# Kernel tuning notes

Measured on AMD Instinct MI355X. Metric: run time of the kernel, lower is better.

Reference implementation:

```python
import jax, jax.numpy as jnp
import numpy as np

B, S, D = 128, 256, 768          # batch, seq (pre-sentinel), encoder dim
ARC, TAG = 500, 100              # arc / tag representation dims
LAYERS, TOPK = 2, 8              # config['gnn_layers'], config['top_k']
SP = S + 1                       # seq_len after head sentinel


def setup_inputs() -> dict:
    key = jax.random.key(0)
    ks = jax.random.split(key, 32)
    sc = 0.02
    inp = {
        'inputs': jax.random.normal(ks[0], (B, S, D), jnp.float32),
        'tag_embeddings': jax.random.randint(ks[1], (B, S), 0, 50),
        'mask': jnp.ones((B, S), jnp.int32),
        'head_indices': jax.random.randint(ks[2], (B, S), 0, S),
        'head_tags': jax.random.randint(ks[3], (B, S), 0, 50),
        # parameters
        'head_sentinel': jax.random.normal(ks[4], (D,), jnp.float32),
        'W_ha': jax.random.normal(ks[5], (D, ARC)) * sc, 'b_ha': jnp.zeros((ARC,)),
        'W_da': jax.random.normal(ks[6], (D, ARC)) * sc, 'b_da': jnp.zeros((ARC,)),
        'W_ht': jax.random.normal(ks[7], (D, TAG)) * sc, 'b_ht': jnp.zeros((TAG,)),
        'W_dt': jax.random.normal(ks[8], (D, TAG)) * sc, 'b_dt': jnp.zeros((TAG,)),
        # bilinear attention: use_input_biases=True -> (ARC+1, ARC+1), plus scalar bias
        'bil_W': jax.random.normal(ks[9], (LAYERS + 1, ARC + 1, ARC + 1)) * sc,
        'bil_b': jnp.zeros((LAYERS + 1,)),
        # GCNConv params (PyG: x @ W, symmetric-normalized aggregate, + bias)
        'c1a_W': jax.random.normal(ks[10], (ARC, ARC)) * sc, 'c1a_b': jnp.zeros((ARC,)),
        'c2a_W': jax.random.normal(ks[11], (ARC, ARC)) * sc, 'c2a_b': jnp.zeros((ARC,)),
        'c1r_W': jax.random.normal(ks[12], (TAG, TAG)) * sc, 'c1r_b': jnp.zeros((TAG,)),
        'c2r_W': jax.random.normal(ks[13], (TAG, TAG)) * sc, 'c2r_b': jnp.zeros((TAG,)),
    }
    return inp


def bilinear_attn(m1, m2, W, b):
    # AllenNLP BilinearMatrixAttention with use_input_biases=True
    ones1 = jnp.ones(m1.shape[:-1] + (1,), m1.dtype)
    m1b = jnp.concatenate([m1, ones1], -1)
    m2b = jnp.concatenate([m2, ones1], -1)
    return jnp.einsum('bie,ef,bjf->bij', m1b, W, m2b) + b


def batch_top_k(probs, k):
    # probs: [B, SP, SP] row-softmaxed; edge j(head)->i(dep) for each row's top-k cols,
    # with global (batched) node indexing.
    vals, idx = jax.lax.top_k(probs, k)                      # [B, SP, k]
    offs = (jnp.arange(B) * SP)[:, None, None]
    src = (idx + offs).reshape(-1)
    dst = (jnp.broadcast_to(jnp.arange(SP)[None, :, None], idx.shape) + offs).reshape(-1)
    return src, dst, vals.reshape(-1)


def gcn_conv(x, src, dst, ew, W, b):
    # PyG GCNConv: x@W, add self-loops (weight 1), sym norm, scatter-add at dst, + bias
    N = x.shape[0]
    x = x @ W
    loop = jnp.arange(N)
    row = jnp.concatenate([src, loop])
    col = jnp.concatenate([dst, loop])
    w = jnp.concatenate([ew, jnp.ones((N,), x.dtype)])
    deg = jax.ops.segment_sum(w, col, num_segments=N)
    dinv = jnp.where(deg > 0, jax.lax.rsqrt(deg), 0.0)
    norm = dinv[row] * w * dinv[col]
    out = jax.ops.segment_sum(x[row] * norm[:, None], col, num_segments=N)
    return out + b


def reference(inputs, tag_embeddings, mask, head_indices, head_tags,
              head_sentinel, W_ha, b_ha, W_da, b_da, W_ht, b_ht, W_dt, b_dt,
              bil_W, bil_b, c1a_W, c1a_b, c2a_W, c2a_b, c1r_W, c1r_b, c2r_W, c2r_b):
    elu = jax.nn.elu
    x = jnp.concatenate([jnp.broadcast_to(head_sentinel, (B, 1, D)), inputs], axis=1)  # [B,SP,D]
    head_arc = elu(x @ W_ha + b_ha)
    dept_arc = elu(x @ W_da + b_da)
    head_tag = elu(x @ W_ht + b_ht)
    dep_tag = elu(x @ W_dt + b_dt)

    def two_conv(feat, W1, b1, W2, b2, src, dst, ew):
        h = gcn_conv(feat.reshape(B * SP, -1), src, dst, ew, W1, b1)
        h = gcn_conv(elu(h), src, dst, ew, W2, b2)
        return h.reshape(B, SP, -1)

    for k in range(LAYERS):
        arc_logits = bilinear_attn(head_arc, dept_arc, bil_W[k], bil_b[k])
        arc_probs = jax.nn.softmax(arc_logits, axis=-1)
        src, dst, ew = batch_top_k(arc_probs, TOPK)
        head_arc = two_conv(head_arc, c1a_W, c1a_b, c2a_W, c2a_b, src, dst, ew)
        dept_arc = two_conv(dept_arc, c1a_W, c1a_b, c2a_W, c2a_b, src, dst, ew)
        head_tag = two_conv(head_tag, c1r_W, c1r_b, c2r_W, c2r_b, src, dst, ew)
        dep_tag = two_conv(dep_tag, c1r_W, c1r_b, c2r_W, c2r_b, src, dst, ew)

    arc_logits = bilinear_attn(head_arc, dept_arc, bil_W[-1], bil_b[-1])
    return arc_logits, head_tag, dep_tag
```

## Files before the change

kernel.cpp:

```cpp
#include <hip/hip_runtime.h>
#include <hip/hip_bf16.h>
#include <math.h>
#include <cstddef>

namespace {

constexpr int kB   = 128;
constexpr int kS   = 256;
constexpr int kD   = 768;
constexpr int kSP  = 257;
constexpr int kN   = kB * kSP;
constexpr int kARC = 500;
constexpr int kTAG = 100;
constexpr int KA   = 512;
constexpr int KT   = 128;

typedef __attribute__((ext_vector_type(8))) short short8;
typedef __attribute__((ext_vector_type(4))) float floatx4;

__device__ __forceinline__ float bfval(__hip_bfloat16 h) { return __bfloat162float(h); }
__device__ __forceinline__ float s2f(short s) {
  unsigned short us = (unsigned short)s;
  __hip_bfloat16 h;
  __builtin_memcpy(&h, &us, 2);
  return __bfloat162float(h);
}
__device__ __forceinline__ void splitf(float x, __hip_bfloat16* h, __hip_bfloat16* l) {
  __hip_bfloat16 hh = __float2bfloat16(x);
  *h = hh;
  *l = __float2bfloat16(x - __bfloat162float(hh));
}

__global__ void detect_dtype_n(const unsigned* __restrict__ raw, int* __restrict__ flag,
                               int nwords) {
  int lane = threadIdx.x;
  int ok = 0, nz = 0;
  if (lane < nwords) {
    unsigned w = raw[lane];
    if (w != 0u) {
      nz = 1;
      int e = (w >> 7) & 0xFF;
      ok = (e >= 90 && e <= 140);
    }
  }
  unsigned long long ball_ok = __ballot(ok);
  unsigned long long ball_nz = __ballot(nz);
  if (lane == 0) {
    int cok = __popcll(ball_ok), cnz = __popcll(ball_nz);
    flag[0] = (cok * 4 >= cnz * 3) ? 1 : 0;
  }
}

__device__ __forceinline__ float rawload(const void* p, size_t i, int bf) {
  return bf ? __bfloat162float(((const __hip_bfloat16*)p)[i]) : ((const float*)p)[i];
}

__global__ void conv_off(const void* __restrict__ src, float* __restrict__ dst,
                         int n, long off, const int* __restrict__ flag) {
  int i = blockIdx.x * 256 + threadIdx.x;
  if (i >= n) return;
  dst[i] = rawload(src, (size_t)off + i, *flag);
}

__global__ void wsplit_t(const void* __restrict__ src, const int* __restrict__ flag,
                         long srcOff, int ldsrc, int K, int N, int Kpad,
                         __hip_bfloat16* __restrict__ Wh, __hip_bfloat16* __restrict__ Wl) {
  long idx = (long)blockIdx.x * 256 + threadIdx.x;
  if (idx >= (long)N * Kpad) return;
  int n = (int)(idx / Kpad), k = (int)(idx % Kpad);
  float v = (k < K) ? rawload(src, (size_t)srcOff + (size_t)k * ldsrc + n, *flag) : 0.f;
  __hip_bfloat16 h, l;
  splitf(v, &h, &l);
  Wh[idx] = h; Wl[idx] = l;
}

constexpr int BM = 128, BN = 128, BK = 32, LDT = 40;

template <int EPI>
__global__ __launch_bounds__(256) void gemm_sp(
    const __hip_bfloat16* __restrict__ Ah, const __hip_bfloat16* __restrict__ Al, int lda,
    const __hip_bfloat16* __restrict__ Bh, const __hip_bfloat16* __restrict__ Bl, int ldb,
    __hip_bfloat16* __restrict__ Ch, __hip_bfloat16* __restrict__ Cl, int ldc,
    int M, int N, int K, const float* __restrict__ bias) {
  __shared__ __hip_bfloat16 sA[2][BM][LDT];
  __shared__ __hip_bfloat16 sB[2][BN][LDT];
  const int tid = threadIdx.x;
  const int lane = tid & 63, wave = tid >> 6;
  const int quad = lane >> 4, l15 = lane & 15;
  const int wm = (wave >> 1) * 64, wn = (wave & 1) * 64;
  const int m0 = blockIdx.x * BM, n0 = blockIdx.y * BN;
  const int srow = tid >> 2, sck = tid & 3;

  floatx4 acc[4][4] = {};
  for (int k0 = 0; k0 < K; k0 += BK) {
#pragma unroll
    for (int half = 0; half < 2; ++half) {
      int r = srow + half * 64;
      {
        int gm = m0 + r;
        short8 vh = {}, vl = {};
        if (gm < M) {
          vh = *(const short8*)(Ah + (size_t)gm * lda + k0 + sck * 8);
          vl = *(const short8*)(Al + (size_t)gm * lda + k0 + sck * 8);
        }
        *(short8*)&sA[0][r][sck * 8] = vh;
        *(short8*)&sA[1][r][sck * 8] = vl;
      }
      {
        int gn = n0 + r;
        short8 vh = {}, vl = {};
        if (gn < N) {
          vh = *(const short8*)(Bh + (size_t)gn * ldb + k0 + sck * 8);
          vl = *(const short8*)(Bl + (size_t)gn * ldb + k0 + sck * 8);
        }
        *(short8*)&sB[0][r][sck * 8] = vh;
        *(short8*)&sB[1][r][sck * 8] = vl;
      }
    }
    __syncthreads();
    short8 a_h[4], a_l[4], b_h[4], b_l[4];
#pragma unroll
    for (int t = 0; t < 4; ++t) {
      a_h[t] = *(const short8*)&sA[0][wm + t * 16 + l15][quad * 8];
      a_l[t] = *(const short8*)&sA[1][wm + t * 16 + l15][quad * 8];
      b_h[t] = *(const short8*)&sB[0][wn + t * 16 + l15][quad * 8];
      b_l[t] = *(const short8*)&sB[1][wn + t * 16 + l15][quad * 8];
    }
#pragma unroll
    for (int mt = 0; mt < 4; ++mt)
#pragma unroll
      for (int nt = 0; nt < 4; ++nt) {
        acc[mt][nt] = __builtin_amdgcn_mfma_f32_16x16x32_bf16(a_h[mt], b_h[nt], acc[mt][nt], 0, 0, 0);
        acc[mt][nt] = __builtin_amdgcn_mfma_f32_16x16x32_bf16(a_h[mt], b_l[nt], acc[mt][nt], 0, 0, 0);
        acc[mt][nt] = __builtin_amdgcn_mfma_f32_16x16x32_bf16(a_l[mt], b_h[nt], acc[mt][nt], 0, 0, 0);
      }
    __syncthreads();
  }
#pragma unroll
  for (int mt = 0; mt < 4; ++mt)
#pragma unroll
    for (int reg = 0; reg < 4; ++reg) {
      int m = m0 + wm + mt * 16 + quad * 4 + reg;
      if (m >= M) continue;
#pragma unroll
      for (int nt = 0; nt < 4; ++nt) {
        int n = n0 + wn + nt * 16 + l15;
        size_t o = (size_t)m * ldc + n;
        if (n < N) {
          float v = acc[mt][nt][reg];
          if (EPI >= 1) v += bias[n];
          if (EPI == 1) v = v > 0.f ? v : expm1f(v);
          __hip_bfloat16 h, l;
          splitf(v, &h, &l);
          Ch[o] = h; Cl[o] = l;
        } else if (n < ldc) {
          Ch[o] = __float2bfloat16(0.f);
          Cl[o] = __float2bfloat16(0.f);
        }
      }
    }
}

__global__ __launch_bounds__(256) void proj_sp(
    const void* __restrict__ inp, const void* __restrict__ sent,
    const int* __restrict__ flag_inp, const int* __restrict__ flag_sent,
    const __hip_bfloat16* __restrict__ Bh, const __hip_bfloat16* __restrict__ Bl,
    __hip_bfloat16* __restrict__ Ch, __hip_bfloat16* __restrict__ Cl, int ldc,
    int M, int N, const float* __restrict__ bias, int g0) {
  __shared__ __hip_bfloat16 sA[2][BM][LDT];
  __shared__ __hip_bfloat16 sB[2][BN][LDT];
  const int bf_i = *flag_inp, bf_s = *flag_sent;
  const int tid = threadIdx.x;
  const int lane = tid & 63, wave = tid >> 6;
  const int quad = lane >> 4, l15 = lane & 15;
  const int wm = (wave >> 1) * 64, wn = (wave & 1) * 64;
  const int m0 = blockIdx.x * BM, n0 = blockIdx.y * BN;
  const int srow = tid >> 2, sck = tid & 3;

  floatx4 acc[4][4] = {};
  for (int k0 = 0; k0 < kD; k0 += BK) {
#pragma unroll
    for (int half = 0; half < 2; ++half) {
      int r = srow + half * 64;
      int gm = m0 + r;
      float v[8] = {0, 0, 0, 0, 0, 0, 0, 0};
      if (gm < M) {
        int b_loc = gm / kSP;
        int rr = gm - b_loc * kSP;
        int kk = k0 + sck * 8;
        if (rr == 0) {
          if (bf_s) {
            short8 s = *(const short8*)((const __hip_bfloat16*)sent + kk);
#pragma unroll
            for (int j = 0; j < 8; ++j) v[j] = s2f(s[j]);
          } else {
            floatx4 a = *(const floatx4*)((const float*)sent + kk);
            floatx4 b = *(const floatx4*)((const float*)sent + kk + 4);
#pragma unroll
            for (int j = 0; j < 4; ++j) { v[j] = a[j]; v[4 + j] = b[j]; }
          }
        } else {
          size_t base = ((size_t)((g0 + b_loc) * kS + (rr - 1))) * kD + kk;
          if (bf_i) {
            short8 s = *(const short8*)((const __hip_bfloat16*)inp + base);
#pragma unroll
            for (int j = 0; j < 8; ++j) v[j] = s2f(s[j]);
          } else {
            floatx4 a = *(const floatx4*)((const float*)inp + base);
            floatx4 b = *(const floatx4*)((const float*)inp + base + 4);
#pragma unroll
            for (int j = 0; j < 4; ++j) { v[j] = a[j]; v[4 + j] = b[j]; }
          }
        }
      }
#pragma unroll
      for (int j = 0; j < 8; ++j) {
        __hip_bfloat16 h, l;
        splitf(v[j], &h, &l);
        sA[0][r][sck * 8 + j] = h;
        sA[1][r][sck * 8 + j] = l;
      }
      {
        int gn = n0 + r;
        short8 vh = {}, vl = {};
        if (gn < N) {
          vh = *(const short8*)(Bh + (size_t)gn * kD + k0 + sck * 8);
          vl = *(const short8*)(Bl + (size_t)gn * kD + k0 + sck * 8);
        }
        *(short8*)&sB[0][r][sck * 8] = vh;
        *(short8*)&sB[1][r][sck * 8] = vl;
      }
    }
    __syncthreads();
    short8 a_h[4], a_l[4], b_h[4], b_l[4];
#pragma unroll
    for (int t = 0; t < 4; ++t) {
      a_h[t] = *(const short8*)&sA[0][wm + t * 16 + l15][quad * 8];
      a_l[t] = *(const short8*)&sA[1][wm + t * 16 + l15][quad * 8];
      b_h[t] = *(const short8*)&sB[0][wn + t * 16 + l15][quad * 8];
      b_l[t] = *(const short8*)&sB[1][wn + t * 16 + l15][quad * 8];
    }
#pragma unroll
    for (int mt = 0; mt < 4; ++mt)
#pragma unroll
      for (int nt = 0; nt < 4; ++nt) {
        acc[mt][nt] = __builtin_amdgcn_mfma_f32_16x16x32_bf16(a_h[mt], b_h[nt], acc[mt][nt], 0, 0, 0);
        acc[mt][nt] = __builtin_amdgcn_mfma_f32_16x16x32_bf16(a_h[mt], b_l[nt], acc[mt][nt], 0, 0, 0);
        acc[mt][nt] = __builtin_amdgcn_mfma_f32_16x16x32_bf16(a_l[mt], b_h[nt], acc[mt][nt], 0, 0, 0);
      }
    __syncthreads();
  }
#pragma unroll
  for (int mt = 0; mt < 4; ++mt)
#pragma unroll
    for (int reg = 0; reg < 4; ++reg) {
      int m = m0 + wm + mt * 16 + quad * 4 + reg;
      if (m >= M) continue;
#pragma unroll
      for (int nt = 0; nt < 4; ++nt) {
        int n = n0 + wn + nt * 16 + l15;
        size_t o = (size_t)m * ldc + n;
        if (n < N) {
          float v = acc[mt][nt][reg] + bias[n];
          v = v > 0.f ? v : expm1f(v);
          __hip_bfloat16 h, l;
          splitf(v, &h, &l);
          Ch[o] = h; Cl[o] = l;
        } else if (n < ldc) {
          Ch[o] = __float2bfloat16(0.f);
          Cl[o] = __float2bfloat16(0.f);
        }
      }
    }
}

__global__ __launch_bounds__(256) void bilnt_sp(
    const __hip_bfloat16* __restrict__ Th, const __hip_bfloat16* __restrict__ Tl,
    const __hip_bfloat16* __restrict__ Fh, const __hip_bfloat16* __restrict__ Fl,
    float* __restrict__ out, const float* __restrict__ bilb, int bidx,
    int g0, int globOut) {
  __shared__ __hip_bfloat16 sA[2][BM][LDT];
  __shared__ __hip_bfloat16 sB[2][BN][LDT];
  const int z = blockIdx.z;
  const int tid = threadIdx.x;
  const int lane = tid & 63, wave = tid >> 6;
  const int quad = lane >> 4, l15 = lane & 15;
  const int wm = (wave >> 1) * 64, wn = (wave & 1) * 64;
  const int m0 = blockIdx.x * BM, n0 = blockIdx.y * BN;
  const int srow = tid >> 2, sck = tid & 3;
  const __hip_bfloat16* Ah = Th + (size_t)z * kSP * KA;
  const __hip_bfloat16* Al = Tl + (size_t)z * kSP * KA;
  const __hip_bfloat16* Bh = Fh + (size_t)z * kSP * KA;
  const __hip_bfloat16* Bl = Fl + (size_t)z * kSP * KA;

  floatx4 acc[4][4] = {};
  for (int k0 = 0; k0 < KA; k0 += BK) {
#pragma unroll
    for (int half = 0; half < 2; ++half) {
      int r = srow + half * 64;
      {
        int gm = m0 + r;
        short8 vh = {}, vl = {};
        if (gm < kSP) {
          vh = *(const short8*)(Ah + (size_t)gm * KA + k0 + sck * 8);
          vl = *(const short8*)(Al + (size_t)gm * KA + k0 + sck * 8);
        }
        *(short8*)&sA[0][r][sck * 8] = vh;
        *(short8*)&sA[1][r][sck * 8] = vl;
      }
      {
        int gn = n0 + r;
        short8 vh = {}, vl = {};
        if (gn < kSP) {
          vh = *(const short8*)(Bh + (size_t)gn * KA + k0 + sck * 8);
          vl = *(const short8*)(Bl + (size_t)gn * KA + k0 + sck * 8);
        }
        *(short8*)&sB[0][r][sck * 8] = vh;
        *(short8*)&sB[1][r][sck * 8] = vl;
      }
    }
    __syncthreads();
    short8 a_h[4], a_l[4], b_h[4], b_l[4];
#pragma unroll
    for (int t = 0; t < 4; ++t) {
      a_h[t] = *(const short8*)&sA[0][wm + t * 16 + l15][quad * 8];
      a_l[t] = *(const short8*)&sA[1][wm + t * 16 + l15][quad * 8];
      b_h[t] = *(const short8*)&sB[0][wn + t * 16 + l15][quad * 8];
      b_l[t] = *(const short8*)&sB[1][wn + t * 16 + l15][quad * 8];
    }
#pragma unroll
    for (int mt = 0; mt < 4; ++mt)
#pragma unroll
      for (int nt = 0; nt < 4; ++nt) {
        acc[mt][nt] = __builtin_amdgcn_mfma_f32_16x16x32_bf16(a_h[mt], b_h[nt], acc[mt][nt], 0, 0, 0);
        acc[mt][nt] = __builtin_amdgcn_mfma_f32_16x16x32_bf16(a_h[mt], b_l[nt], acc[mt][nt], 0, 0, 0);
        acc[mt][nt] = __builtin_amdgcn_mfma_f32_16x16x32_bf16(a_l[mt], b_h[nt], acc[mt][nt], 0, 0, 0);
      }
    __syncthreads();
  }
  const float sb = bilb[bidx];
  const int bb = globOut ? (g0 + z) : z;
#pragma unroll
  for (int mt = 0; mt < 4; ++mt)
// ... 47 lines not shown
      float ov = __shfl_xor(bvv, off);
      int oi = __shfl_xor(bii, off);
      if (ov > bvv || (ov == bvv && oi < bii)) { bvv = ov; bii = oi; }
    }
    float p = expf(bvv - m) * invs;
    degsum += p;
    if (lane == 0) { idx8[row * 8 + t] = rowbase + bii; val8[row * 8 + t] = p; }
#pragma unroll
    for (int q = 0; q < 5; ++q)
      if (c[q] == bii) v[q] = -INFINITY;
  }
  if (lane == 0) dinv[row] = 1.f / sqrtf(1.f + degsum);
}

template <int ELU, int OUTF32>
__global__ __launch_bounds__(256) void gcn_agg_sp(
    const __hip_bfloat16* __restrict__ Yh, const __hip_bfloat16* __restrict__ Yl, int ldy,
    int F,
    const int* __restrict__ idx8, const float* __restrict__ val8,
    const float* __restrict__ dinv,
    const float* __restrict__ bias,
    __hip_bfloat16* __restrict__ Zh, __hip_bfloat16* __restrict__ Zl,
    float* __restrict__ Zf, int ldzf) {
  const int n = blockIdx.x;
  __shared__ float w[9];
  __shared__ int srcs[8];
  const int t = threadIdx.x;
  if (t < 8) {
    int s = idx8[n * 8 + t];
    srcs[t] = s;
    w[t] = dinv[n] * val8[n * 8 + t] * dinv[s];
  } else if (t == 8) {
    float di = dinv[n];
    w[8] = di * di;
  }
  __syncthreads();
  const int lim = OUTF32 ? F : ldy;
  for (int f = t; f < lim; f += blockDim.x) {
    if (!OUTF32 && f >= F) {
      size_t o = (size_t)n * ldy + f;
      Zh[o] = __float2bfloat16(0.f);
      Zl[o] = __float2bfloat16(0.f);
      continue;
    }
    size_t off0 = (size_t)n * ldy + f;
    float acc = w[8] * (bfval(Yh[off0]) + bfval(Yl[off0]));
#pragma unroll
    for (int k = 0; k < 8; ++k) {
      size_t o = (size_t)srcs[k] * ldy + f;
      acc += w[k] * (bfval(Yh[o]) + bfval(Yl[o]));
    }
    acc += bias[f];
    if (ELU) acc = acc > 0.f ? acc : expm1f(acc);
    if (OUTF32) {
      Zf[(size_t)n * ldzf + f] = acc;
    } else {
      __hip_bfloat16 h, l;
      splitf(acc, &h, &l);
      size_t o = (size_t)n * ldy + f;
      Zh[o] = h; Zl[o] = l;
    }
  }
}

}

extern "C" void kernel_launch(void* const* d_in, const int* in_sizes, int n_in,
                              void* d_out, int out_size, void* d_ws, size_t ws_size,
                              hipStream_t stream) {
  (void)out_size;

  const int roleSize[20] = {kB * kS * kD, kD,
                            kD * kARC, kARC, kD * kARC, kARC,
                            kD * kTAG, kTAG, kD * kTAG, kTAG,
                            3 * 501 * 501, 3,
// ... 17 lines not shown
  const void* src_of[20];
  for (int r = 0; r < 20; ++r) src_of[r] = d_in[roleIdx[r]];

  auto need_bytes = [](int GB) -> size_t {
    size_t NG = (size_t)GB * kSP, s = 0;
    auto al = [&](size_t b) { s += (b + 255) & ~(size_t)255; };
    al(256);
    for (int i = 0; i < 4; ++i) al((size_t)kARC * kD * 2);
    for (int i = 0; i < 4; ++i) al((size_t)kTAG * kD * 2);
    al(kARC * 4); al(kARC * 4); al(kTAG * 4); al(kTAG * 4);
    for (int i = 0; i < 6; ++i) al((size_t)501 * KA * 2);
    al(3 * 501 * 4); al(256);
    for (int i = 0; i < 4; ++i) al((size_t)kARC * KA * 2);
    for (int i = 0; i < 4; ++i) al((size_t)kTAG * KT * 2);
    al(kARC * 4); al(kARC * 4); al(kTAG * 4); al(kTAG * 4);
    for (int i = 0; i < 4; ++i) al(NG * KA * 2);
    for (int i = 0; i < 4; ++i) al(NG * KT * 2);
    for (int i = 0; i < 4; ++i) al(NG * KA * 2);
    al(NG * kSP * 4);
    al(NG * 8 * 4); al(NG * 8 * 4); al(NG * 4);
    return s;
  };
  int GB = 1;
  for (int cand : {128, 64, 32, 16, 8, 4, 2, 1})
    if (need_bytes(cand) <= ws_size) { GB = cand; break; }
  const int G = kB / GB;
  const int NG = GB * kSP;
  const int mb = (NG + BM - 1) / BM;

  char* ws = (char*)d_ws;
  size_t off = 0;
  auto alloc = [&](size_t bytes) -> void* {
    void* p = ws + off;
    off += (bytes + 255) & ~(size_t)255;
    return p;
  };
  typedef __hip_bfloat16 bf;
  int* flags = (int*)alloc(256);
  bf *WtHAh = (bf*)alloc((size_t)kARC * kD * 2), *WtHAl = (bf*)alloc((size_t)kARC * kD * 2);
  bf *WtDAh = (bf*)alloc((size_t)kARC * kD * 2), *WtDAl = (bf*)alloc((size_t)kARC * kD * 2);
  bf *WtHTh = (bf*)alloc((size_t)kTAG * kD * 2), *WtHTl = (bf*)alloc((size_t)kTAG * kD * 2);
  bf *WtDTh = (bf*)alloc((size_t)kTAG * kD * 2), *WtDTl = (bf*)alloc((size_t)kTAG * kD * 2);
  float* bha = (float*)alloc(kARC * 4);
  float* bda = (float*)alloc(kARC * 4);
  float* bht = (float*)alloc(kTAG * 4);
  float* bdt = (float*)alloc(kTAG * 4);
  bf* bilWh[3]; bf* bilWl[3];
  for (int k = 0; k < 3; ++k) {
    bilWh[k] = (bf*)alloc((size_t)501 * KA * 2);
    bilWl[k] = (bf*)alloc((size_t)501 * KA * 2);
  }
  float* brow = (float*)alloc(3 * 501 * 4);
  float* bilbf = (float*)alloc(256);
  bf *c1ah = (bf*)alloc((size_t)kARC * KA * 2), *c1al = (bf*)alloc((size_t)kARC * KA * 2);
  bf *c2ah = (bf*)alloc((size_t)kARC * KA * 2), *c2al = (bf*)alloc((size_t)kARC * KA * 2);
  bf *c1rh = (bf*)alloc((size_t)kTAG * KT * 2), *c1rl = (bf*)alloc((size_t)kTAG * KT * 2);
  bf *c2rh = (bf*)alloc((size_t)kTAG * KT * 2), *c2rl = (bf*)alloc((size_t)kTAG * KT * 2);
  float* c1ab = (float*)alloc(kARC * 4);
  float* c2ab = (float*)alloc(kARC * 4);
  float* c1rb = (float*)alloc(kTAG * 4);
  float* c2rb = (float*)alloc(kTAG * 4);
  bf *fHAh = (bf*)alloc((size_t)NG * KA * 2), *fHAl = (bf*)alloc((size_t)NG * KA * 2);
  bf *fDAh = (bf*)alloc((size_t)NG * KA * 2), *fDAl = (bf*)alloc((size_t)NG * KA * 2);
  bf *fHTh = (bf*)alloc((size_t)NG * KT * 2), *fHTl = (bf*)alloc((size_t)NG * KT * 2);
  bf *fDTh = (bf*)alloc((size_t)NG * KT * 2), *fDTl = (bf*)alloc((size_t)NG * KT * 2);
  bf *Yh = (bf*)alloc((size_t)NG * KA * 2), *Yl = (bf*)alloc((size_t)NG * KA * 2);
  bf *Zh = (bf*)alloc((size_t)NG * KA * 2), *Zl = (bf*)alloc((size_t)NG * KA * 2);
  float* logits = (float*)alloc((size_t)NG * kSP * 4);
  int*   idx8 = (int*)alloc((size_t)NG * 8 * 4);
  float* val8 = (float*)alloc((size_t)NG * 8 * 4);
  float* dinv = (float*)alloc((size_t)NG * 4);

  for (int r = 0; r < 20; ++r) {
    int n = roleSize[r];
    int nwords = n / 4; if (nwords < 1) nwords = 1; if (nwords > 64) nwords = 64;
    detect_dtype_n<<<1, 64, 0, stream>>>((const unsigned*)src_of[r], flags + r, nwords);
  }
  auto cvt = [&](int role, float* dst, int n, long o) {
    conv_off<<<(n + 255) / 256, 256, 0, stream>>>(src_of[role], dst, n, o, flags + role);
  };
  cvt(3, bha, kARC, 0); cvt(5, bda, kARC, 0); cvt(7, bht, kTAG, 0); cvt(9, bdt, kTAG, 0);
  cvt(11, bilbf, 3, 0);
// ... 10 lines not shown
  for (int k = 0; k < 3; ++k) {
    wsp(10, (long)k * 501 * 501, 501, 500, 501, KA, bilWh[k], bilWl[k]);
    cvt(10, brow + k * 501, 501, (long)k * 501 * 501 + 500 * 501);
  }
  wsp(12, 0, kARC, kARC, kARC, KA, c1ah, c1al);
  wsp(14, 0, kARC, kARC, kARC, KA, c2ah, c2al);
  wsp(16, 0, kTAG, kTAG, kTAG, KT, c1rh, c1rl);
  wsp(18, 0, kTAG, kTAG, kTAG, KT, c2rh, c2rl);

  float* outp = (float*)d_out;
  const size_t arc_elems = (size_t)kB * kSP * kSP;

  for (int g = 0; g < G; ++g) {
    const int g0 = g * GB;

    proj_sp<<<dim3(mb, 4), 256, 0, stream>>>(src_of[0], src_of[1], flags + 0, flags + 1,
                                             WtHAh, WtHAl, fHAh, fHAl, KA, NG, kARC, bha, g0);
    proj_sp<<<dim3(mb, 4), 256, 0, stream>>>(src_of[0], src_of[1], flags + 0, flags + 1,
                                             WtDAh, WtDAl, fDAh, fDAl, KA, NG, kARC, bda, g0);
    proj_sp<<<dim3(mb, 1), 256, 0, stream>>>(src_of[0], src_of[1], flags + 0, flags + 1,
                                             WtHTh, WtHTl, fHTh, fHTl, KT, NG, kTAG, bht, g0);
    proj_sp<<<dim3(mb, 1), 256, 0, stream>>>(src_of[0], src_of[1], flags + 0, flags + 1,
                                             WtDTh, WtDTl, fDTh, fDTl, KT, NG, kTAG, bdt, g0);

    for (int k = 0; k < 2; ++k) {
      gemm_sp<2><<<dim3(mb, 4), 256, 0, stream>>>(fHAh, fHAl, KA, bilWh[k], bilWl[k], KA,
                                                  Yh, Yl, KA, NG, 501, KA, brow + k * 501);
      bilnt_sp<<<dim3(3, 3, GB), 256, 0, stream>>>(Yh, Yl, fDAh, fDAl, logits, bilbf, k, g0, 0);
      softmax_topk<<<NG, 64, 0, stream>>>(logits, idx8, val8, dinv);

      bf* fh[2] = {fHAh, fDAh};
      bf* fl[2] = {fHAl, fDAl};
      for (int ff = 0; ff < 2; ++ff) {
        gemm_sp<0><<<dim3(mb, 4), 256, 0, stream>>>(fh[ff], fl[ff], KA, c1ah, c1al, KA,
                                                    Yh, Yl, KA, NG, kARC, KA, nullptr);
        gcn_agg_sp<1, 0><<<NG, 256, 0, stream>>>(Yh, Yl, KA, kARC, idx8, val8, dinv, c1ab,
                                                 Zh, Zl, nullptr, 0);
        gemm_sp<0><<<dim3(mb, 4), 256, 0, stream>>>(Zh, Zl, KA, c2ah, c2al, KA,
                                                    Yh, Yl, KA, NG, kARC, KA, nullptr);
        gcn_agg_sp<0, 0><<<NG, 256, 0, stream>>>(Yh, Yl, KA, kARC, idx8, val8, dinv, c2ab,
                                                 fh[ff], fl[ff], nullptr, 0);
      }
      bf* th[2] = {fHTh, fDTh};
      bf* tl[2] = {fHTl, fDTl};
      for (int ff = 0; ff < 2; ++ff) {
        gemm_sp<0><<<dim3(mb, 1), 256, 0, stream>>>(th[ff], tl[ff], KT, c1rh, c1rl, KT,
                                                    Zh, Zl, KT, NG, kTAG, KT, nullptr);
        gcn_agg_sp<1, 0><<<NG, 256, 0, stream>>>(Zh, Zl, KT, kTAG, idx8, val8, dinv, c1rb,
                                                 Yh, Yl, nullptr, 0);
        gemm_sp<0><<<dim3(mb, 1), 256, 0, stream>>>(Yh, Yl, KT, c2rh, c2rl, KT,
                                                    Zh, Zl, KT, NG, kTAG, KT, nullptr);
        if (k == 1) {
          float* dst = outp + arc_elems + (ff == 1 ? (size_t)kN * kTAG : 0)
                       + (size_t)g0 * kSP * kTAG;
          gcn_agg_sp<0, 1><<<NG, 256, 0, stream>>>(Zh, Zl, KT, kTAG, idx8, val8, dinv, c2rb,
                                                   nullptr, nullptr, dst, kTAG);
        } else {
          gcn_agg_sp<0, 0><<<NG, 256, 0, stream>>>(Zh, Zl, KT, kTAG, idx8, val8, dinv, c2rb,
                                                   th[ff], tl[ff], nullptr, 0);
        }
      }
    }

    gemm_sp<2><<<dim3(mb, 4), 256, 0, stream>>>(fHAh, fHAl, KA, bilWh[2], bilWl[2], KA,
                                                Yh, Yl, KA, NG, 501, KA, brow + 2 * 501);
    bilnt_sp<<<dim3(3, 3, GB), 256, 0, stream>>>(Yh, Yl, fDAh, fDAl, outp, bilbf, 2, g0, 1);
  }
}
```

Before: 3.163 ms.

## Use direct global-to-LDS loads, pre-split inputs, and fp32 intermediates for GCN

GEMM and bilinear kernels now stage tiles with global_load_lds (16-byte direct-to-LDS) into unpadded shared arrays, replacing register round-trips and bounds zeroing with clamped row pointers. The fused projection kernel is replaced by a one-time xsplit pass that converts the input to hi/lo bf16, followed by the generic GEMM. GCN transform GEMMs write fp32 outputs consumed by a rewritten aggregation kernel, and the tag-path aggregation uses 64-thread blocks. The unpadded LDS layout may cause bank conflicts on fragment reads, and the extra split buffer adds memory traffic.

```diff
diff --git a/kernel.cpp b/kernel.cpp
--- a/kernel.cpp
+++ b/kernel.cpp
@@ -17,18 +17,25 @@
 
 typedef __attribute__((ext_vector_type(8))) short short8;
 typedef __attribute__((ext_vector_type(4))) float floatx4;
-
-__device__ __forceinline__ float bfval(__hip_bfloat16 h) { return __bfloat162float(h); }
-__device__ __forceinline__ float s2f(short s) {
-  unsigned short us = (unsigned short)s;
-  __hip_bfloat16 h;
-  __builtin_memcpy(&h, &us, 2);
-  return __bfloat162float(h);
-}
-__device__ __forceinline__ void splitf(float x, __hip_bfloat16* h, __hip_bfloat16* l) {
-  __hip_bfloat16 hh = __float2bfloat16(x);
+typedef __attribute__((ext_vector_type(2))) float floatx2;
+typedef __attribute__((ext_vector_type(4))) unsigned short ushort4v;
+typedef __attribute__((ext_vector_type(2))) unsigned short ushort2v;
+typedef __hip_bfloat16 bf;
+
+__device__ __forceinline__ float bfval(bf h) { return __bfloat162float(h); }
+__device__ __forceinline__ unsigned short bfbits(bf h) {
+  unsigned short u; __builtin_memcpy(&u, &h, 2); return u;
+}
+__device__ __forceinline__ void splitf(float x, bf* h, bf* l) {
+  bf hh = __float2bfloat16(x);
   *h = hh;
   *l = __float2bfloat16(x - __bfloat162float(hh));
+}
+
+__device__ __forceinline__ void gload16(const bf* g, bf* l) {
+  __builtin_amdgcn_global_load_lds(
+      (const __attribute__((address_space(1))) void*)g,
+      (__attribute__((address_space(3))) void*)l, 16, 0, 0);
 }
 
 __global__ void detect_dtype_n(const unsigned* __restrict__ raw, int* __restrict__ flag,
@@ -51,8 +58,8 @@
   }
 }
 
-__device__ __forceinline__ float rawload(const void* p, size_t i, int bf) {
-  return bf ? __bfloat162float(((const __hip_bfloat16*)p)[i]) : ((const float*)p)[i];
+__device__ __forceinline__ float rawload(const void* p, size_t i, int bfm) {
+  return bfm ? __bfloat162float(((const bf*)p)[i]) : ((const float*)p)[i];
 }
 
 __global__ void conv_off(const void* __restrict__ src, float* __restrict__ dst,
@@ -64,67 +71,109 @@
 
 __global__ void wsplit_t(const void* __restrict__ src, const int* __restrict__ flag,
                          long srcOff, int ldsrc, int K, int N, int Kpad,
-                         __hip_bfloat16* __restrict__ Wh, __hip_bfloat16* __restrict__ Wl) {
+                         bf* __restrict__ Wh, bf* __restrict__ Wl) {
   long idx = (long)blockIdx.x * 256 + threadIdx.x;
   if (idx >= (long)N * Kpad) return;
   int n = (int)(idx / Kpad), k = (int)(idx % Kpad);
   float v = (k < K) ? rawload(src, (size_t)srcOff + (size_t)k * ldsrc + n, *flag) : 0.f;
-  __hip_bfloat16 h, l;
+  bf h, l;
   splitf(v, &h, &l);
   Wh[idx] = h; Wl[idx] = l;
 }
 
-constexpr int BM = 128, BN = 128, BK = 32, LDT = 40;
-
-template <int EPI>
+__global__ void xsplit(const void* __restrict__ inp, const void* __restrict__ sent,
+                       const int* __restrict__ fi, const int* __restrict__ fs,
+                       bf* __restrict__ xh, bf* __restrict__ xl, int g0, int NG) {
+  long idx = (long)blockIdx.x * 256 + threadIdx.x;
+  long tot = (long)NG * (kD / 4);
+  if (idx >= tot) return;
+  int n = (int)(idx / (kD / 4));
+  int k = (int)(idx % (kD / 4)) * 4;
+  int b = n / kSP, r = n - b * kSP;
+  const void* src;
+  size_t base;
+  int bfm;
+  if (r == 0) { src = sent; base = (size_t)k; bfm = *fs; }
+  else {
+    src = inp;
+    base = ((size_t)((g0 + b) * kS + (r - 1))) * kD + k;
+    bfm = *fi;
+  }
+  float v[4];
+  if (bfm) {
+    ushort4v s = *(const ushort4v*)((const unsigned short*)src + base);
+#pragma unroll
+    for (int j = 0; j < 4; ++j) {
+      bf h; unsigned short u = s[j];
+      __builtin_memcpy(&h, &u, 2);
+      v[j] = __bfloat162float(h);
+    }
+  } else {
+    floatx4 f4 = *(const floatx4*)((const float*)src + base);
+#pragma unroll
+    for (int j = 0; j < 4; ++j) v[j] = f4[j];
+  }
+  ushort4v h4, l4;
+#pragma unroll
+  for (int j = 0; j < 4; ++j) {
+    bf h, l;
+    splitf(v[j], &h, &l);
+    h4[j] = bfbits(h); l4[j] = bfbits(l);
+  }
+  size_t o = (size_t)n * kD + k;
+  *(ushort4v*)((unsigned short*)xh + o) = h4;
+  *(ushort4v*)((unsigned short*)xl + o) = l4;
+}
+
+constexpr int BM = 128, BN = 128, BK = 32;
+
+template <int EPI, int OUTF32>
 __global__ __launch_bounds__(256) void gemm_sp(
-    const __hip_bfloat16* __restrict__ Ah, const __hip_bfloat16* __restrict__ Al, int lda,
-    const __hip_bfloat16* __restrict__ Bh, const __hip_bfloat16* __restrict__ Bl, int ldb,
-    __hip_bfloat16* __restrict__ Ch, __hip_bfloat16* __restrict__ Cl, int ldc,
+    const bf* __restrict__ Ah, const bf* __restrict__ Al, int lda,
+    const bf* __restrict__ Bh, const bf* __restrict__ Bl, int ldb,
+    bf* __restrict__ Ch, bf* __restrict__ Cl, float* __restrict__ Cf, int ldc,
     int M, int N, int K, const float* __restrict__ bias) {
-  __shared__ __hip_bfloat16 sA[2][BM][LDT];
-  __shared__ __hip_bfloat16 sB[2][BN][LDT];
+  __shared__ bf sAh[BM][BK];
+  __shared__ bf sAl[BM][BK];
+  __shared__ bf sBh[BN][BK];
+  __shared__ bf sBl[BN][BK];
   const int tid = threadIdx.x;
   const int lane = tid & 63, wave = tid >> 6;
   const int quad = lane >> 4, l15 = lane & 15;
   const int wm = (wave >> 1) * 64, wn = (wave & 1) * 64;
   const int m0 = blockIdx.x * BM, n0 = blockIdx.y * BN;
-  const int srow = tid >> 2, sck = tid & 3;
+  const int lrow = lane >> 2, lkof = (lane & 3) * 8;
+
+  const bf *pAh[2], *pAl[2], *pBh[2], *pBl[2];
+#pragma unroll
+  for (int jj = 0; jj < 2; ++jj) {
+    int rb = wave * 32 + jj * 16;
+    int gm = m0 + rb + lrow; if (gm > M - 1) gm = M - 1;
+    int gn = n0 + rb + lrow; if (gn > N - 1) gn = N - 1;
+    pAh[jj] = Ah + (size_t)gm * lda + lkof;
+    pAl[jj] = Al + (size_t)gm * lda + lkof;
+    pBh[jj] = Bh + (size_t)gn * ldb + lkof;
+    pBl[jj] = Bl + (size_t)gn * ldb + lkof;
+  }
 
   floatx4 acc[4][4] = {};
   for (int k0 = 0; k0 < K; k0 += BK) {
 #pragma unroll
-    for (int half = 0; half < 2; ++half) {
-      int r = srow + half * 64;
-      {
-        int gm = m0 + r;
-        short8 vh = {}, vl = {};
-        if (gm < M) {
-          vh = *(const short8*)(Ah + (size_t)gm * lda + k0 + sck * 8);
-          vl = *(const short8*)(Al + (size_t)gm * lda + k0 + sck * 8);
-        }
-        *(short8*)&sA[0][r][sck * 8] = vh;
-        *(short8*)&sA[1][r][sck * 8] = vl;
-      }
-      {
-        int gn = n0 + r;
-        short8 vh = {}, vl = {};
-        if (gn < N) {
-          vh = *(const short8*)(Bh + (size_t)gn * ldb + k0 + sck * 8);
-          vl = *(const short8*)(Bl + (size_t)gn * ldb + k0 + sck * 8);
-        }
-        *(short8*)&sB[0][r][sck * 8] = vh;
-        *(short8*)&sB[1][r][sck * 8] = vl;
-      }
+    for (int jj = 0; jj < 2; ++jj) {
+      const int rb = wave * 32 + jj * 16;
+      gload16(pAh[jj] + k0, &sAh[rb][0]);
+      gload16(pAl[jj] + k0, &sAl[rb][0]);
+      gload16(pBh[jj] + k0, &sBh[rb][0]);
+      gload16(pBl[jj] + k0, &sBl[rb][0]);
     }
     __syncthreads();
     short8 a_h[4], a_l[4], b_h[4], b_l[4];
 #pragma unroll
     for (int t = 0; t < 4; ++t) {
-      a_h[t] = *(const short8*)&sA[0][wm + t * 16 + l15][quad * 8];
-      a_l[t] = *(const short8*)&sA[1][wm + t * 16 + l15][quad * 8];
-      b_h[t] = *(const short8*)&sB[0][wn + t * 16 + l15][quad * 8];
-      b_l[t] = *(const short8*)&sB[1][wn + t * 16 + l15][quad * 8];
+      a_h[t] = *(const short8*)&sAh[wm + t * 16 + l15][quad * 8];
+      a_l[t] = *(const short8*)&sAl[wm + t * 16 + l15][quad * 8];
+      b_h[t] = *(const short8*)&sBh[wn + t * 16 + l15][quad * 8];
+      b_l[t] = *(const short8*)&sBl[wn + t * 16 + l15][quad * 8];
     }
 #pragma unroll
     for (int mt = 0; mt < 4; ++mt)
@@ -145,188 +194,82 @@
 #pragma unroll
       for (int nt = 0; nt < 4; ++nt) {
         int n = n0 + wn + nt * 16 + l15;
-        size_t o = (size_t)m * ldc + n;
-        if (n < N) {
-          float v = acc[mt][nt][reg];
-          if (EPI >= 1) v += bias[n];
-          if (EPI == 1) v = v > 0.f ? v : expm1f(v);
-          __hip_bfloat16 h, l;
-          splitf(v, &h, &l);
-          Ch[o] = h; Cl[o] = l;
-        } else if (n < ldc) {
-          Ch[o] = __float2bfloat16(0.f);
-          Cl[o] = __float2bfloat16(0.f);
-        }
-      }
-    }
-}
-
-__global__ __launch_bounds__(256) void proj_sp(
-    const void* __restrict__ inp, const void* __restrict__ sent,
-    const int* __restrict__ flag_inp, const int* __restrict__ flag_sent,
-    const __hip_bfloat16* __restrict__ Bh, const __hip_bfloat16* __restrict__ Bl,
-    __hip_bfloat16* __restrict__ Ch, __hip_bfloat16* __restrict__ Cl, int ldc,
-    int M, int N, const float* __restrict__ bias, int g0) {
-  __shared__ __hip_bfloat16 sA[2][BM][LDT];
-  __shared__ __hip_bfloat16 sB[2][BN][LDT];
-  const int bf_i = *flag_inp, bf_s = *flag_sent;
-  const int tid = threadIdx.x;
-  const int lane = tid & 63, wave = tid >> 6;
-  const int quad = lane >> 4, l15 = lane & 15;
-  const int wm = (wave >> 1) * 64, wn = (wave & 1) * 64;
-  const int m0 = blockIdx.x * BM, n0 = blockIdx.y * BN;
-  const int srow = tid >> 2, sck = tid & 3;
-
-  floatx4 acc[4][4] = {};
-  for (int k0 = 0; k0 < kD; k0 += BK) {
-#pragma unroll
-    for (int half = 0; half < 2; ++half) {
-      int r = srow + half * 64;
-      int gm = m0 + r;
-      float v[8] = {0, 0, 0, 0, 0, 0, 0, 0};
-      if (gm < M) {
-        int b_loc = gm / kSP;
-        int rr = gm - b_loc * kSP;
-        int kk = k0 + sck * 8;
-        if (rr == 0) {
-          if (bf_s) {
-            short8 s = *(const short8*)((const __hip_bfloat16*)sent + kk);
-#pragma unroll
-            for (int j = 0; j < 8; ++j) v[j] = s2f(s[j]);
-          } else {
-            floatx4 a = *(const floatx4*)((const float*)sent + kk);
-            floatx4 b = *(const floatx4*)((const float*)sent + kk + 4);
-#pragma unroll
-            for (int j = 0; j < 4; ++j) { v[j] = a[j]; v[4 + j] = b[j]; }
+        if (OUTF32) {
+          if (n < N) {
+            float v = acc[mt][nt][reg];
+            if (EPI >= 1) v += bias[n];
+            if (EPI == 1) v = v > 0.f ? v : expm1f(v);
+            Cf[(size_t)m * ldc + n] = v;
           }
         } else {
-          size_t base = ((size_t)((g0 + b_loc) * kS + (rr - 1))) * kD + kk;
-          if (bf_i) {
-            short8 s = *(const short8*)((const __hip_bfloat16*)inp + base);
-#pragma unroll
-            for (int j = 0; j < 8; ++j) v[j] = s2f(s[j]);
-          } else {
-            floatx4 a = *(const floatx4*)((const float*)inp + base);
-            floatx4 b = *(const floatx4*)((const float*)inp + base + 4);
-#pragma unroll
-            for (int j = 0; j < 4; ++j) { v[j] = a[j]; v[4 + j] = b[j]; }
+          size_t o = (size_t)m * ldc + n;
+          if (n < N) {
+            float v = acc[mt][nt][reg];
+            if (EPI >= 1) v += bias[n];
+            if (EPI == 1) v = v > 0.f ? v : expm1f(v);
+            bf h, l;
+            splitf(v, &h, &l);
+            Ch[o] = h; Cl[o] = l;
+          } else if (n < ldc) {
+            Ch[o] = __float2bfloat16(0.f);
+            Cl[o] = __float2bfloat16(0.f);
           }
         }
       }
-#pragma unroll
-      for (int j = 0; j < 8; ++j) {
-        __hip_bfloat16 h, l;
-        splitf(v[j], &h, &l);
-        sA[0][r][sck * 8 + j] = h;
-        sA[1][r][sck * 8 + j] = l;
-      }
-      {
-        int gn = n0 + r;
-        short8 vh = {}, vl = {};
-        if (gn < N) {
-          vh = *(const short8*)(Bh + (size_t)gn * kD + k0 + sck * 8);
-          vl = *(const short8*)(Bl + (size_t)gn * kD + k0 + sck * 8);
-        }
-        *(short8*)&sB[0][r][sck * 8] = vh;
-        *(short8*)&sB[1][r][sck * 8] = vl;
-      }
-    }
-    __syncthreads();
-    short8 a_h[4], a_l[4], b_h[4], b_l[4];
-#pragma unroll
-    for (int t = 0; t < 4; ++t) {
-      a_h[t] = *(const short8*)&sA[0][wm + t * 16 + l15][quad * 8];
-      a_l[t] = *(const short8*)&sA[1][wm + t * 16 + l15][quad * 8];
-      b_h[t] = *(const short8*)&sB[0][wn + t * 16 + l15][quad * 8];
-      b_l[t] = *(const short8*)&sB[1][wn + t * 16 + l15][quad * 8];
-    }
-#pragma unroll
-    for (int mt = 0; mt < 4; ++mt)
-#pragma unroll
-      for (int nt = 0; nt < 4; ++nt) {
-        acc[mt][nt] = __builtin_amdgcn_mfma_f32_16x16x32_bf16(a_h[mt], b_h[nt], acc[mt][nt], 0, 0, 0);
-        acc[mt][nt] = __builtin_amdgcn_mfma_f32_16x16x32_bf16(a_h[mt], b_l[nt], acc[mt][nt], 0, 0, 0);
-        acc[mt][nt] = __builtin_amdgcn_mfma_f32_16x16x32_bf16(a_l[mt], b_h[nt], acc[mt][nt], 0, 0, 0);
-      }
-    __syncthreads();
-  }
-#pragma unroll
-  for (int mt = 0; mt < 4; ++mt)
-#pragma unroll
-    for (int reg = 0; reg < 4; ++reg) {
-      int m = m0 + wm + mt * 16 + quad * 4 + reg;
-      if (m >= M) continue;
-#pragma unroll
-      for (int nt = 0; nt < 4; ++nt) {
-        int n = n0 + wn + nt * 16 + l15;
-        size_t o = (size_t)m * ldc + n;
-        if (n < N) {
-          float v = acc[mt][nt][reg] + bias[n];
-          v = v > 0.f ? v : expm1f(v);
-          __hip_bfloat16 h, l;
-          splitf(v, &h, &l);
-          Ch[o] = h; Cl[o] = l;
-        } else if (n < ldc) {
-          Ch[o] = __float2bfloat16(0.f);
-          Cl[o] = __float2bfloat16(0.f);
-        }
-      }
     }
 }
 
 __global__ __launch_bounds__(256) void bilnt_sp(
-    const __hip_bfloat16* __restrict__ Th, const __hip_bfloat16* __restrict__ Tl,
-    const __hip_bfloat16* __restrict__ Fh, const __hip_bfloat16* __restrict__ Fl,
+    const bf* __restrict__ Th, const bf* __restrict__ Tl,
+    const bf* __restrict__ Fh, const bf* __restrict__ Fl,
     float* __restrict__ out, const float* __restrict__ bilb, int bidx,
     int g0, int globOut) {
-  __shared__ __hip_bfloat16 sA[2][BM][LDT];
-  __shared__ __hip_bfloat16 sB[2][BN][LDT];
+  __shared__ bf sAh[BM][BK];
+  __shared__ bf sAl[BM][BK];
+  __shared__ bf sBh[BN][BK];
+  __shared__ bf sBl[BN][BK];
   const int z = blockIdx.z;
   const int tid = threadIdx.x;
   const int lane = tid & 63, wave = tid >> 6;
   const int quad = lane >> 4, l15 = lane & 15;
   const int wm = (wave >> 1) * 64, wn = (wave & 1) * 64;
   const int m0 = blockIdx.x * BM, n0 = blockIdx.y * BN;
-  const int srow = tid >> 2, sck = tid & 3;
-  const __hip_bfloat16* Ah = Th + (size_t)z * kSP * KA;
-  const __hip_bfloat16* Al = Tl + (size_t)z * kSP * KA;
-  const __hip_bfloat16* Bh = Fh + (size_t)z * kSP * KA;
-  const __hip_bfloat16* Bl = Fl + (size_t)z * kSP * KA;
+  const int lrow = lane >> 2, lkof = (lane & 3) * 8;
+  const bf* Ah = Th + (size_t)z * kSP * KA;
+  const bf* Al = Tl + (size_t)z * kSP * KA;
+  const bf* Bh = Fh + (size_t)z * kSP * KA;
+  const bf* Bl = Fl + (size_t)z * kSP * KA;
+
+  const bf *pAh[2], *pAl[2], *pBh[2], *pBl[2];
+#pragma unroll
+  for (int jj = 0; jj < 2; ++jj) {
+    int rb = wave * 32 + jj * 16;
+    int gm = m0 + rb + lrow; if (gm > kSP - 1) gm = kSP - 1;
+    int gn = n0 + rb + lrow; if (gn > kSP - 1) gn = kSP - 1;
+    pAh[jj] = Ah + (size_t)gm * KA + lkof;
+    pAl[jj] = Al + (size_t)gm * KA + lkof;
+    pBh[jj] = Bh + (size_t)gn * KA + lkof;
+    pBl[jj] = Bl + (size_t)gn * KA + lkof;
+  }
 
   floatx4 acc[4][4] = {};
   for (int k0 = 0; k0 < KA; k0 += BK) {
 #pragma unroll
-    for (int half = 0; half < 2; ++half) {
-      int r = srow + half * 64;
-      {
-        int gm = m0 + r;
-        short8 vh = {}, vl = {};
-        if (gm < kSP) {
-          vh = *(const short8*)(Ah + (size_t)gm * KA + k0 + sck * 8);
-          vl = *(const short8*)(Al + (size_t)gm * KA + k0 + sck * 8);
-        }
-        *(short8*)&sA[0][r][sck * 8] = vh;
-        *(short8*)&sA[1][r][sck * 8] = vl;
-      }
-      {
-        int gn = n0 + r;
-        short8 vh = {}, vl = {};
-        if (gn < kSP) {
-          vh = *(const short8*)(Bh + (size_t)gn * KA + k0 + sck * 8);
-          vl = *(const short8*)(Bl + (size_t)gn * KA + k0 + sck * 8);
-        }
-        *(short8*)&sB[0][r][sck * 8] = vh;
-        *(short8*)&sB[1][r][sck * 8] = vl;
-      }
+    for (int jj = 0; jj < 2; ++jj) {
+      const int rb = wave * 32 + jj * 16;
+      gload16(pAh[jj] + k0, &sAh[rb][0]);
+      gload16(pAl[jj] + k0, &sAl[rb][0]);
+      gload16(pBh[jj] + k0, &sBh[rb][0]);
+      gload16(pBl[jj] + k0, &sBl[rb][0]);
     }
     __syncthreads();
     short8 a_h[4], a_l[4], b_h[4], b_l[4];
 #pragma unroll
     for (int t = 0; t < 4; ++t) {
-      a_h[t] = *(const short8*)&sA[0][wm + t * 16 + l15][quad * 8];
-      a_l[t] = *(const short8*)&sA[1][wm + t * 16 + l15][quad * 8];
-      b_h[t] = *(const short8*)&sB[0][wn + t * 16 + l15][quad * 8];
-      b_l[t] = *(const short8*)&sB[1][wn + t * 16 + l15][quad * 8];
+      a_h[t] = *(const short8*)&sAh[wm + t * 16 + l15][quad * 8];
+      a_l[t] = *(const short8*)&sAl[wm + t * 16 + l15][quad * 8];
+      b_h[t] = *(const short8*)&sBh[wn + t * 16 + l15][quad * 8];
+      b_l[t] = *(const short8*)&sBl[wn + t * 16 + l15][quad * 8];
     }
 #pragma unroll
     for (int mt = 0; mt < 4; ++mt)
@@ -404,14 +347,11 @@
 }
 
 template <int ELU, int OUTF32>
-__global__ __launch_bounds__(256) void gcn_agg_sp(
-    const __hip_bfloat16* __restrict__ Yh, const __hip_bfloat16* __restrict__ Yl, int ldy,
-    int F,
-    const int* __restrict__ idx8, const float* __restrict__ val8,
-    const float* __restrict__ dinv,
-    const float* __restrict__ bias,
-    __hip_bfloat16* __restrict__ Zh, __hip_bfloat16* __restrict__ Zl,
-    float* __restrict__ Zf, int ldzf) {
+__global__ void gcn_agg(const float* __restrict__ Y, int ldy, int F,
+                        const int* __restrict__ idx8, const float* __restrict__ val8,
+                        const float* __restrict__ dinv, const float* __restrict__ bias,
+                        bf* __restrict__ Zh, bf* __restrict__ Zl,
+                        float* __restrict__ Zf, int ldzf) {
   const int n = blockIdx.x;
   __shared__ float w[9];
   __shared__ int srcs[8];
@@ -426,29 +366,39 @@
   }
   __syncthreads();
   const int lim = OUTF32 ? F : ldy;
-  for (int f = t; f < lim; f += blockDim.x) {
+  for (int f = t * 2; f < lim; f += (int)blockDim.x * 2) {
+    size_t on = (size_t)n * ldy + f;
     if (!OUTF32 && f >= F) {
-      size_t o = (size_t)n * ldy + f;
-      Zh[o] = __float2bfloat16(0.f);
-      Zl[o] = __float2bfloat16(0.f);
+      ushort2v zz = {0, 0};
+      *(ushort2v*)((unsigned short*)Zh + on) = zz;
+      *(ushort2v*)((unsigned short*)Zl + on) = zz;
       continue;
     }
-    size_t off0 = (size_t)n * ldy + f;
-    float acc = w[8] * (bfval(Yh[off0]) + bfval(Yl[off0]));
-#pragma unroll
-    for (int k = 0; k < 8; ++k) {
-      size_t o = (size_t)srcs[k] * ldy + f;
-      acc += w[k] * (bfval(Yh[o]) + bfval(Yl[o]));
-    }
-    acc += bias[f];
-    if (ELU) acc = acc > 0.f ? acc : expm1f(acc);
+    floatx2 y0 = *(const floatx2*)(Y + on);
+    float a0 = w[8] * y0[0], a1 = w[8] * y0[1];
+#pragma unroll
+    for (int e = 0; e < 8; ++e) {
+      floatx2 ys = *(const floatx2*)(Y + (size_t)srcs[e] * ldy + f);
+      a0 += w[e] * ys[0];
+      a1 += w[e] * ys[1];
+    }
+    a0 += bias[f];
+    a1 += bias[f + 1];
+    if (ELU) {
+      a0 = a0 > 0.f ? a0 : expm1f(a0);
+      a1 = a1 > 0.f ? a1 : expm1f(a1);
+    }
     if (OUTF32) {
-      Zf[(size_t)n * ldzf + f] = acc;
+      floatx2 o = {a0, a1};
+      *(floatx2*)(Zf + (size_t)n * ldzf + f) = o;
     } else {
-      __hip_bfloat16 h, l;
-      splitf(acc, &h, &l);
-      size_t o = (size_t)n * ldy + f;
-      Zh[o] = h; Zl[o] = l;
+      bf h0, l0, h1, l1;
+      splitf(a0, &h0, &l0);
+      splitf(a1, &h1, &l1);
+      ushort2v hv = {bfbits(h0), bfbits(h1)};
+      ushort2v lv = {bfbits(l0), bfbits(l1)};
+      *(ushort2v*)((unsigned short*)Zh + on) = hv;
+      *(ushort2v*)((unsigned short*)Zl + on) = lv;
     }
   }
 }
@@ -496,9 +446,11 @@
     for (int i = 0; i < 4; ++i) al((size_t)kARC * KA * 2);
     for (int i = 0; i < 4; ++i) al((size_t)kTAG * KT * 2);
     al(kARC * 4); al(kARC * 4); al(kTAG * 4); al(kTAG * 4);
+    al(NG * kD * 2); al(NG * kD * 2);
     for (int i = 0; i < 4; ++i) al(NG * KA * 2);
     for (int i = 0; i < 4; ++i) al(NG * KT * 2);
-    for (int i = 0; i < 4; ++i) al(NG * KA * 2);
+    al(NG * KA * 2); al(NG * KA * 2);
+    al(NG * KA * 4);
     al(NG * kSP * 4);
     al(NG * 8 * 4); al(NG * 8 * 4); al(NG * 4);
     return s;
@@ -517,7 +469,6 @@
     off += (bytes + 255) & ~(size_t)255;
     return p;
   };
-  typedef __hip_bfloat16 bf;
   int* flags = (int*)alloc(256);
   bf *WtHAh = (bf*)alloc((size_t)kARC * kD * 2), *WtHAl = (bf*)alloc((size_t)kARC * kD * 2);
   bf *WtDAh = (bf*)alloc((size_t)kARC * kD * 2), *WtDAl = (bf*)alloc((size_t)kARC * kD * 2);
@@ -542,12 +493,13 @@
   float* c2ab = (float*)alloc(kARC * 4);
   float* c1rb = (float*)alloc(kTAG * 4);
   float* c2rb = (float*)alloc(kTAG * 4);
+  bf *xh = (bf*)alloc((size_t)NG * kD * 2), *xl = (bf*)alloc((size_t)NG * kD * 2);
   bf *fHAh = (bf*)alloc((size_t)NG * KA * 2), *fHAl = (bf*)alloc((size_t)NG * KA * 2);
   bf *fDAh = (bf*)alloc((size_t)NG * KA * 2), *fDAl = (bf*)alloc((size_t)NG * KA * 2);
   bf *fHTh = (bf*)alloc((size_t)NG * KT * 2), *fHTl = (bf*)alloc((size_t)NG * KT * 2);
   bf *fDTh = (bf*)alloc((size_t)NG * KT * 2), *fDTl = (bf*)alloc((size_t)NG * KT * 2);
   bf *Yh = (bf*)alloc((size_t)NG * KA * 2), *Yl = (bf*)alloc((size_t)NG * KA * 2);
-  bf *Zh = (bf*)alloc((size_t)NG * KA * 2), *Zl = (bf*)alloc((size_t)NG * KA * 2);
+  float* Yf = (float*)alloc((size_t)NG * KA * 4);
   float* logits = (float*)alloc((size_t)NG * kSP * 4);
   int*   idx8 = (int*)alloc((size_t)NG * 8 * 4);
   float* val8 = (float*)alloc((size_t)NG * 8 * 4);
@@ -588,56 +540,67 @@
   for (int g = 0; g < G; ++g) {
     const int g0 = g * GB;
 
-    proj_sp<<<dim3(mb, 4), 256, 0, stream>>>(src_of[0], src_of[1], flags + 0, flags + 1,
-                                             WtHAh, WtHAl, fHAh, fHAl, KA, NG, kARC, bha, g0);
-    proj_sp<<<dim3(mb, 4), 256, 0, stream>>>(src_of[0], src_of[1], flags + 0, flags + 1,
-                                             WtDAh, WtDAl, fDAh, fDAl, KA, NG, kARC, bda, g0);
-    proj_sp<<<dim3(mb, 1), 256, 0, stream>>>(src_of[0], src_of[1], flags + 0, flags + 1,
-                                             WtHTh, WtHTl, fHTh, fHTl, KT, NG, kTAG, bht, g0);
-    proj_sp<<<dim3(mb, 1), 256, 0, stream>>>(src_of[0], src_of[1], flags + 0, flags + 1,
-                                             WtDTh, WtDTl, fDTh, fDTl, KT, NG, kTAG, bdt, g0);
+    {
+      long tot = (long)NG * (kD / 4);
+      xsplit<<<(int)((tot + 255) / 256), 256, 0, stream>>>(
+          src_of[0], src_of[1], flags + 0, flags + 1, xh, xl, g0, NG);
+    }
+    gemm_sp<1, 0><<<dim3(mb, 4), 256, 0, stream>>>(xh, xl, kD, WtHAh, WtHAl, kD,
+                                                   fHAh, fHAl, nullptr, KA, NG, kARC, kD, bha);
+    gemm_sp<1, 0><<<dim3(mb, 4), 256, 0, stream>>>(xh, xl, kD, WtDAh, WtDAl, kD,
+                                                   fDAh, fDAl, nullptr, KA, NG, kARC, kD, bda);
+    gemm_sp<1, 0><<<dim3(mb, 1), 256, 0, stream>>>(xh, xl, kD, WtHTh, WtHTl, kD,
+                                                   fHTh, fHTl, nullptr, KT, NG, kTAG, kD, bht);
+    gemm_sp<1, 0><<<dim3(mb, 1), 256, 0, stream>>>(xh, xl, kD, WtDTh, WtDTl, kD,
+                                                   fDTh, fDTl, nullptr, KT, NG, kTAG, kD, bdt);
 
     for (int k = 0; k < 2; ++k) {
-      gemm_sp<2><<<dim3(mb, 4), 256, 0, stream>>>(fHAh, fHAl, KA, bilWh[k], bilWl[k], KA,
-                                                  Yh, Yl, KA, NG, 501, KA, brow + k * 501);
+      gemm_sp<2, 0><<<dim3(mb, 4), 256, 0, stream>>>(fHAh, fHAl, KA, bilWh[k], bilWl[k], KA,
+                                                     Yh, Yl, nullptr, KA, NG, 501, KA,
+                                                     brow + k * 501);
       bilnt_sp<<<dim3(3, 3, GB), 256, 0, stream>>>(Yh, Yl, fDAh, fDAl, logits, bilbf, k, g0, 0);
       softmax_topk<<<NG, 64, 0, stream>>>(logits, idx8, val8, dinv);
 
       bf* fh[2] = {fHAh, fDAh};
       bf* fl[2] = {fHAl, fDAl};
       for (int ff = 0; ff < 2; ++ff) {
-        gemm_sp<0><<<dim3(mb, 4), 256, 0, stream>>>(fh[ff], fl[ff], KA, c1ah, c1al, KA,
-                                                    Yh, Yl, KA, NG, kARC, KA, nullptr);
-        gcn_agg_sp<1, 0><<<NG, 256, 0, stream>>>(Yh, Yl, KA, kARC, idx8, val8, dinv, c1ab,
-                                                 Zh, Zl, nullptr, 0);
-        gemm_sp<0><<<dim3(mb, 4), 256, 0, stream>>>(Zh, Zl, KA, c2ah, c2al, KA,
-                                                    Yh, Yl, KA, NG, kARC, KA, nullptr);
-        gcn_agg_sp<0, 0><<<NG, 256, 0, stream>>>(Yh, Yl, KA, kARC, idx8, val8, dinv, c2ab,
-                                                 fh[ff], fl[ff], nullptr, 0);
+        gemm_sp<0, 1><<<dim3(mb, 4), 256, 0, stream>>>(fh[ff], fl[ff], KA, c1ah, c1al, KA,
+                                                       nullptr, nullptr, Yf, KA, NG, kARC, KA,
+                                                       nullptr);
+        gcn_agg<1, 0><<<NG, 256, 0, stream>>>(Yf, KA, kARC, idx8, val8, dinv, c1ab,
+                                              Yh, Yl, nullptr, 0);
+        gemm_sp<0, 1><<<dim3(mb, 4), 256, 0, stream>>>(Yh, Yl, KA, c2ah, c2al, KA,
+                                                       nullptr, nullptr, Yf, KA, NG, kARC, KA,
+                                                       nullptr);
+        gcn_agg<0, 0><<<NG, 256, 0, stream>>>(Yf, KA, kARC, idx8, val8, dinv, c2ab,
+                                              fh[ff], fl[ff], nullptr, 0);
       }
       bf* th[2] = {fHTh, fDTh};
       bf* tl[2] = {fHTl, fDTl};
       for (int ff = 0; ff < 2; ++ff) {
-        gemm_sp<0><<<dim3(mb, 1), 256, 0, stream>>>(th[ff], tl[ff], KT, c1rh, c1rl, KT,
-                                                    Zh, Zl, KT, NG, kTAG, KT, nullptr);
-        gcn_agg_sp<1, 0><<<NG, 256, 0, stream>>>(Zh, Zl, KT, kTAG, idx8, val8, dinv, c1rb,
-                                                 Yh, Yl, nullptr, 0);
-        gemm_sp<0><<<dim3(mb, 1), 256, 0, stream>>>(Yh, Yl, KT, c2rh, c2rl, KT,
-                                                    Zh, Zl, KT, NG, kTAG, KT, nullptr);
+        gemm_sp<0, 1><<<dim3(mb, 1), 256, 0, stream>>>(th[ff], tl[ff], KT, c1rh, c1rl, KT,
+                                                       nullptr, nullptr, Yf, KT, NG, kTAG, KT,
+                                                       nullptr);
+        gcn_agg<1, 0><<<NG, 64, 0, stream>>>(Yf, KT, kTAG, idx8, val8, dinv, c1rb,
+                                             Yh, Yl, nullptr, 0);
+        gemm_sp<0, 1><<<dim3(mb, 1), 256, 0, stream>>>(Yh, Yl, KT, c2rh, c2rl, KT,
+                                                       nullptr, nullptr, Yf, KT, NG, kTAG, KT,
+                                                       nullptr);
         if (k == 1) {
           float* dst = outp + arc_elems + (ff == 1 ? (size_t)kN * kTAG : 0)
                        + (size_t)g0 * kSP * kTAG;
-          gcn_agg_sp<0, 1><<<NG, 256, 0, stream>>>(Zh, Zl, KT, kTAG, idx8, val8, dinv, c2rb,
-                                                   nullptr, nullptr, dst, kTAG);
+          gcn_agg<0, 1><<<NG, 64, 0, stream>>>(Yf, KT, kTAG, idx8, val8, dinv, c2rb,
+                                               nullptr, nullptr, dst, kTAG);
         } else {
-          gcn_agg_sp<0, 0><<<NG, 256, 0, stream>>>(Zh, Zl, KT, kTAG, idx8, val8, dinv, c2rb,
-                                                   th[ff], tl[ff], nullptr, 0);
+          gcn_agg<0, 0><<<NG, 64, 0, stream>>>(Yf, KT, kTAG, idx8, val8, dinv, c2rb,
+                                               th[ff], tl[ff], nullptr, 0);
         }
       }
     }
 
-    gemm_sp<2><<<dim3(mb, 4), 256, 0, stream>>>(fHAh, fHAl, KA, bilWh[2], bilWl[2], KA,
-                                                Yh, Yl, KA, NG, 501, KA, brow + 2 * 501);
+    gemm_sp<2, 0><<<dim3(mb, 4), 256, 0, stream>>>(fHAh, fHAl, KA, bilWh[2], bilWl[2], KA,
+                                                   Yh, Yl, nullptr, KA, NG, 501, KA,
+                                                   brow + 2 * 501);
     bilnt_sp<<<dim3(3, 3, GB), 256, 0, stream>>>(Yh, Yl, fDAh, fDAl, outp, bilbf, 2, g0, 1);
   }
 }
```

New measurement: 3.405 ms. 1.08x slower.
